# Kernel optimization log

Measured on AMD Instinct MI355X. Metric: run time of the kernel, lower is better.

The kernel has to match this reference:

```python
import jax, jax.numpy as jnp
import numpy as np

EPS = 1e-16  # PyG softmax eps
NEG_SLOPE = 0.2


def _gat_conv(x, W, att_src, att_dst, bias, src, dst, num_nodes, heads, ch, concat):
    # add self loops (PyG default add_self_loops=True)
    loop = jnp.arange(num_nodes, dtype=src.dtype)
    src = jnp.concatenate([src, loop])
    dst = jnp.concatenate([dst, loop])

    h = (x @ W).reshape(num_nodes, heads, ch)          # [N,H,C]
    a_src = jnp.sum(h * att_src, axis=-1)              # [N,H]
    a_dst = jnp.sum(h * att_dst, axis=-1)              # [N,H]

    e = a_src[src] + a_dst[dst]                        # [E,H]
    e = jnp.where(e > 0, e, NEG_SLOPE * e)             # leaky_relu

    # segment softmax over edges grouped by destination node
    m = jax.ops.segment_max(e, dst, num_segments=num_nodes)
    e = jnp.exp(e - m[dst])
    s = jax.ops.segment_sum(e, dst, num_segments=num_nodes)
    alpha = e / (s[dst] + EPS)                          # [E,H]

    msg = h[src] * alpha[:, :, None]                    # [E,H,C]
    out = jax.ops.segment_sum(msg, dst, num_segments=num_nodes)  # [N,H,C]

    if concat:
        out = out.reshape(num_nodes, heads * ch)
    else:
        out = out.mean(axis=1)
    return out + bias


def setup_inputs() -> dict:
    key = jax.random.key(0)
    ks = jax.random.split(key, 12)
    N, E = 50000, 800000
    C_in, C_hid, C_out, H = 128, 32, 64, 8

    x = jax.random.normal(ks[0], (N, C_in), dtype=jnp.float32)
    edge_index = jax.random.randint(ks[1], (2, E), 0, N, dtype=jnp.int64)
    edge_weight = jax.random.uniform(ks[2], (E,), dtype=jnp.float32)

    g = lambda k, shape, fan: jax.random.normal(k, shape, dtype=jnp.float32) * (1.0 / np.sqrt(fan))
    W1 = g(ks[3], (C_in, H * C_hid), C_in)
    att_src1 = g(ks[4], (H, C_hid), C_hid)
    att_dst1 = g(ks[5], (H, C_hid), C_hid)
    bias1 = jnp.zeros((H * C_hid,), dtype=jnp.float32)
    W2 = g(ks[6], (H * C_hid, C_out), H * C_hid)
    att_src2 = g(ks[7], (1, C_out), C_out)
    att_dst2 = g(ks[8], (1, C_out), C_out)
    bias2 = jnp.zeros((C_out,), dtype=jnp.float32)

    return {"x": x, "edge_index": edge_index, "edge_weight": edge_weight,
            "W1": W1, "att_src1": att_src1, "att_dst1": att_dst1, "bias1": bias1,
            "W2": W2, "att_src2": att_src2, "att_dst2": att_dst2, "bias2": bias2}


def reference(x, edge_index, edge_weight, W1, att_src1, att_dst1, bias1,
              W2, att_src2, att_dst2, bias2):
    N = x.shape[0]
    src, dst = edge_index[0], edge_index[1]
    # edge_weight is ignored: GATConv has edge_dim=None, so edge_attr contributes nothing
    h = _gat_conv(x, W1, att_src1, att_dst1, bias1, src, dst, N, 8, 32, concat=True)
    h = jax.nn.elu(h)
    out = _gat_conv(h, W2, att_src2, att_dst2, bias2, src, dst, N, 1, 64, concat=False)
    return out
```

## Files before the change

kernel.cpp:

```cpp
#include <hip/hip_runtime.h>
#include <hip/hip_fp16.h>
#include <math.h>


#define LEAKY(e) ((e) > 0.f ? (e) : 0.2f * (e))
#define CAP 64
#define NPART 4
#define NPB 12500
#define NPW 6250
#define CS 8192

struct __align__(8) H4 { __half2 a, b; };

typedef _Float16 half8 __attribute__((ext_vector_type(8)));
typedef float f32x4 __attribute__((ext_vector_type(4)));

__global__ __launch_bounds__(256) void k1_kernel(
    const int* __restrict__ ei, unsigned* __restrict__ Hg,
    const float* __restrict__ x,
    const float* __restrict__ W1, _Float16* __restrict__ h1h,
    const float* __restrict__ att_src1, const float* __restrict__ att_dst1,
    float* __restrict__ a_src1, float* __restrict__ a_dst1, int N, int E,
    int B, int hblocks) {
  __shared__ __align__(16) unsigned sraw[8704];
  int t = threadIdx.x, b = blockIdx.x;
  if (b < hblocks) {
    int chunk = b >> 2, p = b & 3;
    for (int i = t; i < NPW; i += 256) sraw[i] = 0u;
    __syncthreads();
    int base = chunk * CS;
    int pbase = p * NPB;
    if ((E & 3) == 0) {
      for (int j = 0; j < CS; j += 1024) {
        int idx = base + j + t * 4;
        if (idx < E) {
          int4 dv = *(const int4*)(ei + E + idx);
          unsigned dl;
          dl = (unsigned)(dv.x - pbase);
          if (dl < NPB) atomicAdd(&sraw[dl >> 1], 1u << ((dl & 1) * 16));
          dl = (unsigned)(dv.y - pbase);
          if (dl < NPB) atomicAdd(&sraw[dl >> 1], 1u << ((dl & 1) * 16));
          dl = (unsigned)(dv.z - pbase);
          if (dl < NPB) atomicAdd(&sraw[dl >> 1], 1u << ((dl & 1) * 16));
          dl = (unsigned)(dv.w - pbase);
          if (dl < NPB) atomicAdd(&sraw[dl >> 1], 1u << ((dl & 1) * 16));
        }
      }
    } else {
      for (int j = 0; j < CS; j += 256) {
        int idx = base + j + t;
        if (idx < E) {
          int d = ei[E + idx];
          unsigned dl = (unsigned)(d - pbase);
          if (dl < NPB) atomicAdd(&sraw[dl >> 1], 1u << ((dl & 1) * 16));
        }
      }
    }
    __syncthreads();
    unsigned* Hs = Hg + (size_t)(p * B + chunk) * NPW;
    for (int i = t; i < NPW; i += 256) Hs[i] = sraw[i];
    return;
  }
  _Float16* Bs = (_Float16*)sraw;
  int bx = b - hblocks;
  int cb = bx & 1;
  int c0 = cb * 128;
  int w = t >> 6, l = t & 63;
  int lm = l & 15, lq = l >> 4;
  {
    int n = t & 127;
    int kw = t >> 7;
#pragma unroll 8
    for (int i = 0; i < 64; i++) {
      int k = i * 2 + kw;
      Bs[n * 136 + k] = (_Float16)W1[k * 256 + c0 + n];
    }
  }
  __syncthreads();
  int m0 = (bx >> 1) * 128 + w * 32;
  int ra = m0 + lm;      if (ra > N - 1) ra = N - 1;
  int rb = m0 + 16 + lm; if (rb > N - 1) rb = N - 1;
  f32x4 acc[2][8];
#pragma unroll
  for (int mt = 0; mt < 2; mt++)
#pragma unroll
    for (int nt = 0; nt < 8; nt++) acc[mt][nt] = (f32x4){0.f, 0.f, 0.f, 0.f};
  for (int k0 = 0; k0 < 128; k0 += 32) {
    const float* pa = x + (size_t)ra * 128 + k0 + lq * 8;
    const float* pb = x + (size_t)rb * 128 + k0 + lq * 8;
    float4 u0 = *(const float4*)pa, u1 = *(const float4*)(pa + 4);
    float4 w0 = *(const float4*)pb, w1 = *(const float4*)(pb + 4);
    half8 a0, a1;
    a0[0] = (_Float16)u0.x; a0[1] = (_Float16)u0.y;
    a0[2] = (_Float16)u0.z; a0[3] = (_Float16)u0.w;
    a0[4] = (_Float16)u1.x; a0[5] = (_Float16)u1.y;
    a0[6] = (_Float16)u1.z; a0[7] = (_Float16)u1.w;
    a1[0] = (_Float16)w0.x; a1[1] = (_Float16)w0.y;
    a1[2] = (_Float16)w0.z; a1[3] = (_Float16)w0.w;
    a1[4] = (_Float16)w1.x; a1[5] = (_Float16)w1.y;
    a1[6] = (_Float16)w1.z; a1[7] = (_Float16)w1.w;
#pragma unroll
    for (int nt = 0; nt < 8; nt++) {
      half8 bv = *(const half8*)(Bs + (nt * 16 + lm) * 136 + k0 + lq * 8);
      acc[0][nt] = __builtin_amdgcn_mfma_f32_16x16x32_f16(a0, bv, acc[0][nt], 0, 0, 0);
      acc[1][nt] = __builtin_amdgcn_mfma_f32_16x16x32_f16(a1, bv, acc[1][nt], 0, 0, 0);
    }
  }
  float as_[8], ad_[8];
#pragma unroll
  for (int nt = 0; nt < 8; nt++) {
    as_[nt] = att_src1[c0 + nt * 16 + lm];
    ad_[nt] = att_dst1[c0 + nt * 16 + lm];
  }
#pragma unroll
  for (int mt = 0; mt < 2; mt++) {
#pragma unroll
    for (int i = 0; i < 4; i++) {
      int gr = m0 + mt * 16 + lq * 4 + i;
      bool ok = gr < N;
      if (ok) {
#pragma unroll
        for (int nt = 0; nt < 8; nt++)
          h1h[(size_t)gr * 256 + c0 + nt * 16 + lm] = (_Float16)acc[mt][nt][i];
      }
      float ph[4], qh[4];
#pragma unroll
      for (int hb = 0; hb < 4; hb++) {
        ph[hb] = acc[mt][2 * hb][i] * as_[2 * hb] +
                 acc[mt][2 * hb + 1][i] * as_[2 * hb + 1];
        qh[hb] = acc[mt][2 * hb][i] * ad_[2 * hb] +
                 acc[mt][2 * hb + 1][i] * ad_[2 * hb + 1];
      }
#pragma unroll
      for (int o = 1; o < 16; o <<= 1) {
#pragma unroll
        for (int hb = 0; hb < 4; hb++) {
          ph[hb] += __shfl_xor(ph[hb], o, 64);
          qh[hb] += __shfl_xor(qh[hb], o, 64);
        }
      }
      if (lm == 0 && ok) {
        int h0 = cb * 4;
#pragma unroll
        for (int hb = 0; hb < 4; hb++) {
          a_src1[(size_t)gr * 8 + h0 + hb] = ph[hb];
          a_dst1[(size_t)gr * 8 + h0 + hb] = qh[hb];
        }
      }
    }
  }
}

__global__ __launch_bounds__(256) void prefix_kernel(
    unsigned* __restrict__ Hg, int* __restrict__ deg,
    int* __restrict__ csr_src, int N, int B) {
  int wid = blockIdx.x * 256 + threadIdx.x;
  if (wid >= NPART * NPW) return;
  int p = wid / NPW, w0 = wid - p * NPW;
  unsigned* Hp = Hg + (size_t)p * B * NPW + w0;
  unsigned lo = 0, hi = 0;
  int b = 0;
  for (; b + 4 <= B; b += 4) {
    unsigned v0 = Hp[(size_t)(b + 0) * NPW];
    unsigned v1 = Hp[(size_t)(b + 1) * NPW];
    unsigned v2 = Hp[(size_t)(b + 2) * NPW];
    unsigned v3 = Hp[(size_t)(b + 3) * NPW];
    Hp[(size_t)(b + 0) * NPW] = lo | (hi << 16); lo += v0 & 0xffffu; hi += v0 >> 16;
    Hp[(size_t)(b + 1) * NPW] = lo | (hi << 16); lo += v1 & 0xffffu; hi += v1 >> 16;
    Hp[(size_t)(b + 2) * NPW] = lo | (hi << 16); lo += v2 & 0xffffu; hi += v2 >> 16;
    Hp[(size_t)(b + 3) * NPW] = lo | (hi << 16); lo += v3 & 0xffffu; hi += v3 >> 16;
  }
  for (; b < B; b++) {
    unsigned v = Hp[(size_t)b * NPW];
    Hp[(size_t)b * NPW] = lo | (hi << 16);
    lo += v & 0xffffu;
    hi += v >> 16;
  }
  int d0 = p * NPB + 2 * w0, d1 = d0 + 1;
  if (d0 < N) { deg[d0] = (int)lo; csr_src[(size_t)d0 * CAP] = d0; }
  if (d1 < N) { deg[d1] = (int)hi; csr_src[(size_t)d1 * CAP] = d1; }
}

__global__ __launch_bounds__(256) void scatter_kernel(
    const int* __restrict__ ei, const unsigned* __restrict__ Hg,
    int* __restrict__ csr_src, int E, int B) {
  __shared__ unsigned cnt[NPW];
  int t = threadIdx.x, b = blockIdx.x;
  int chunk = b >> 2, p = b & 3;
  const unsigned* Hs = Hg + (size_t)(p * B + chunk) * NPW;
  for (int i = t; i < NPW; i += 256) cnt[i] = Hs[i];
  __syncthreads();
  int base = chunk * CS;
  int pbase = p * NPB;
  if ((E & 3) == 0) {
    for (int j = 0; j < CS; j += 1024) {
      int idx = base + j + t * 4;
      if (idx < E) {
        int4 sv = *(const int4*)(ei + idx);
        int4 dv = *(const int4*)(ei + E + idx);
        int ss[4] = {sv.x, sv.y, sv.z, sv.w};
        int dd[4] = {dv.x, dv.y, dv.z, dv.w};
#pragma unroll
        for (int q = 0; q < 4; q++) {
          unsigned dl = (unsigned)(dd[q] - pbase);
          if (dl < NPB) {
            unsigned sh = (dl & 1) * 16;
            unsigned old = atomicAdd(&cnt[dl >> 1], 1u << sh);
            int slot = 1 + (int)((old >> sh) & 0xffffu);
            if (slot < CAP) csr_src[(size_t)dd[q] * CAP + slot] = ss[q];
          }
        }
      }
    }
  } else {
    for (int j = 0; j < CS; j += 256) {
      int idx = base + j + t;
      if (idx < E) {
        int s = ei[idx];
        int d = ei[E + idx];
        unsigned dl = (unsigned)(d - pbase);
        if (dl < NPB) {
          unsigned sh = (dl & 1) * 16;
          unsigned old = atomicAdd(&cnt[dl >> 1], 1u << sh);
          int slot = 1 + (int)((old >> sh) & 0xffffu);
          if (slot < CAP) csr_src[(size_t)d * CAP + slot] = s;
        }
      }
    }
  }
}

__global__ __launch_bounds__(256) void agg1_kernel(
    const int* __restrict__ deg, const int* __restrict__ csr_src,
    const float* __restrict__ a_src1, const float* __restrict__ a_dst1,
    const __half* __restrict__ h1h, const float* __restrict__ bias,
    _Float16* __restrict__ h_act, int n) {
  int w = threadIdx.x >> 6, l = threadIdx.x & 63;
  int d = blockIdx.x * 4 + w;
  if (d >= n) return;
  int cnt = deg[d] + 1;
  if (cnt > CAP) cnt = CAP;
  const int* sp = csr_src + (size_t)d * CAP;
  int hh = l >> 3;
  float adst = a_dst1[(size_t)d * 8 + hh];
  float4 acc = make_float4(0.f, 0.f, 0.f, 0.f);
  float p = 0.f;
  int i = 0;
  for (; i + 8 <= cnt; i += 8) {
    int s[8];
#pragma unroll
    for (int j = 0; j < 8; j++) s[j] = sp[i + j];
    int sm = sp[i + (l & 7)];
    float e = a_src1[(size_t)sm * 8 + hh] + adst;
    e = LEAKY(e);
    float ex = __expf(e);
    H4 v[8];
#pragma unroll
    for (int j = 0; j < 8; j++)
      v[j] = *(const H4*)(h1h + (size_t)s[j] * 256 + 4 * l);
    float xv[8];
#pragma unroll
    for (int j = 0; j < 8; j++) {
      xv[j] = __shfl(ex, (l & 56) + j, 64);
      p += xv[j];
    }
#pragma unroll
    for (int j = 0; j < 8; j++) {
      float2 p0 = __half22float2(v[j].a), p1 = __half22float2(v[j].b);
      acc.x = fmaf(p0.x, xv[j], acc.x);
      acc.y = fmaf(p0.y, xv[j], acc.y);
      acc.z = fmaf(p1.x, xv[j], acc.z);
      acc.w = fmaf(p1.y, xv[j], acc.w);
    }
  }
  for (; i < cnt; i++) {
    int s = sp[i];
    float e = a_src1[(size_t)s * 8 + hh] + adst;
    e = LEAKY(e);
    float a = __expf(e);
    p += a;
    H4 v = *(const H4*)(h1h + (size_t)s * 256 + 4 * l);
    float2 p0 = __half22float2(v.a), p1 = __half22float2(v.b);
    acc.x = fmaf(p0.x, a, acc.x);
    acc.y = fmaf(p0.y, a, acc.y);
    acc.z = fmaf(p1.x, a, acc.z);
    acc.w = fmaf(p1.y, a, acc.w);
  }
  float rinv = 1.f / (p + 1e-16f);
  float4 b = *(const float4*)(bias + 4 * l);
  float ox = fmaf(acc.x, rinv, b.x), oy = fmaf(acc.y, rinv, b.y);
  float oz = fmaf(acc.z, rinv, b.z), ow = fmaf(acc.w, rinv, b.w);
  ox = ox > 0.f ? ox : expm1f(ox);
  oy = oy > 0.f ? oy : expm1f(oy);
  oz = oz > 0.f ? oz : expm1f(oz);
  ow = ow > 0.f ? ow : expm1f(ow);
  H4 hv;
  hv.a = __floats2half2_rn(ox, oy);
  hv.b = __floats2half2_rn(oz, ow);
  *(H4*)(h_act + (size_t)d * 256 + 4 * l) = hv;
}

__global__ __launch_bounds__(256) void gemm2_kernel(
    const _Float16* __restrict__ h_act, const float* __restrict__ W2,
    _Float16* __restrict__ h2h, const float* __restrict__ att_src2,
    const float* __restrict__ att_dst2, float* __restrict__ a_src2,
    float* __restrict__ a_dst2, int N) {
  __shared__ _Float16 Bs[64 * 264];
  int t = threadIdx.x;
  int w = t >> 6, l = t & 63;
  int lm = l & 15, lq = l >> 4;
  {
    int n = t & 63;
    int kw = t >> 6;
#pragma unroll 8
    for (int i = 0; i < 64; i++) {
      int k = i * 4 + kw;
      Bs[n * 264 + k] = (_Float16)W2[k * 64 + n];
    }
  }
  __syncthreads();
  const int K = 256;
  int m0 = blockIdx.x * 128 + w * 32;
  int ra = m0 + lm;      if (ra > N - 1) ra = N - 1;
  int rb = m0 + 16 + lm; if (rb > N - 1) rb = N - 1;
  f32x4 acc[2][4];
#pragma unroll
  for (int mt = 0; mt < 2; mt++)
#pragma unroll
    for (int nt = 0; nt < 4; nt++) acc[mt][nt] = (f32x4){0.f, 0.f, 0.f, 0.f};
  for (int k0 = 0; k0 < K; k0 += 32) {
    half8 a0 = *(const half8*)(h_act + (size_t)ra * K + k0 + lq * 8);
    half8 a1 = *(const half8*)(h_act + (size_t)rb * K + k0 + lq * 8);
    half8 b0 = *(const half8*)(Bs + (0 + lm) * 264 + k0 + lq * 8);
    half8 b1 = *(const half8*)(Bs + (16 + lm) * 264 + k0 + lq * 8);
    half8 b2 = *(const half8*)(Bs + (32 + lm) * 264 + k0 + lq * 8);
    half8 b3 = *(const half8*)(Bs + (48 + lm) * 264 + k0 + lq * 8);
    acc[0][0] = __builtin_amdgcn_mfma_f32_16x16x32_f16(a0, b0, acc[0][0], 0, 0, 0);
    acc[0][1] = __builtin_amdgcn_mfma_f32_16x16x32_f16(a0, b1, acc[0][1], 0, 0, 0);
    acc[0][2] = __builtin_amdgcn_mfma_f32_16x16x32_f16(a0, b2, acc[0][2], 0, 0, 0);
    acc[0][3] = __builtin_amdgcn_mfma_f32_16x16x32_f16(a0, b3, acc[0][3], 0, 0, 0);
    acc[1][0] = __builtin_amdgcn_mfma_f32_16x16x32_f16(a1, b0, acc[1][0], 0, 0, 0);
    acc[1][1] = __builtin_amdgcn_mfma_f32_16x16x32_f16(a1, b1, acc[1][1], 0, 0, 0);
    acc[1][2] = __builtin_amdgcn_mfma_f32_16x16x32_f16(a1, b2, acc[1][2], 0, 0, 0);
    acc[1][3] = __builtin_amdgcn_mfma_f32_16x16x32_f16(a1, b3, acc[1][3], 0, 0, 0);
  }
  float as_[4], ad_[4];
#pragma unroll
  for (int nt = 0; nt < 4; nt++) {
    as_[nt] = att_src2[nt * 16 + lm];
    ad_[nt] = att_dst2[nt * 16 + lm];
  }
#pragma unroll
  for (int mt = 0; mt < 2; mt++) {
#pragma unroll
    for (int i = 0; i < 4; i++) {
      int gr = m0 + mt * 16 + lq * 4 + i;
      bool ok = gr < N;
      if (ok) {
#pragma unroll
        for (int nt = 0; nt < 4; nt++)
          h2h[(size_t)gr * 64 + nt * 16 + lm] = (_Float16)acc[mt][nt][i];
      }
      float p0 = acc[mt][0][i] * as_[0] + acc[mt][1][i] * as_[1];
      float p1 = acc[mt][2][i] * as_[2] + acc[mt][3][i] * as_[3];
      float q0 = acc[mt][0][i] * ad_[0] + acc[mt][1][i] * ad_[1];
      float q1 = acc[mt][2][i] * ad_[2] + acc[mt][3][i] * ad_[3];
#pragma unroll
      for (int o = 1; o < 16; o <<= 1) {
        p0 += __shfl_xor(p0, o, 64);
        p1 += __shfl_xor(p1, o, 64);
        q0 += __shfl_xor(q0, o, 64);
        q1 += __shfl_xor(q1, o, 64);
      }
      if (lm == 0 && ok) {
        a_src2[gr] = p0 + p1;
        a_dst2[gr] = q0 + q1;
      }
    }
  }
}

__global__ __launch_bounds__(256) void agg2_kernel(
    const int* __restrict__ deg, const int* __restrict__ csr_src,
    const float* __restrict__ a_src2, const float* __restrict__ a_dst2,
    const __half* __restrict__ h2h, const float* __restrict__ bias,
    float* __restrict__ out, int n) {
  int w = threadIdx.x >> 6, l = threadIdx.x & 63;
  int d = blockIdx.x * 4 + w;
  if (d >= n) return;
  int cnt = deg[d] + 1;
  if (cnt > CAP) cnt = CAP;
  const int* sp = csr_src + (size_t)d * CAP;
  float adst = a_dst2[d];
  int e2 = l >> 5;
  int c2 = (l & 31) * 2;
  float2 acc = make_float2(0.f, 0.f);
  float p = 0.f;
  int i = 0;
  for (; i + 16 <= cnt; i += 16) {
    int s[8];
#pragma unroll
    for (int j = 0; j < 8; j++) s[j] = sp[i + j * 2 + e2];
    int sm = sp[i + (l & 15)];
    float e = a_src2[sm] + adst;
    e = LEAKY(e);
    float ex = __expf(e);
    __half2 v[8];
#pragma unroll
    for (int j = 0; j < 8; j++)
      v[j] = *(const __half2*)(h2h + (size_t)s[j] * 64 + c2);
    float xv[8];
#pragma unroll
    for (int j = 0; j < 8; j++) {
      xv[j] = __shfl(ex, (l & 48) + j * 2 + e2, 64);
      p += xv[j];
    }
#pragma unroll
    for (int j = 0; j < 8; j++) {
      float2 f = __half22float2(v[j]);
      acc.x = fmaf(f.x, xv[j], acc.x);
      acc.y = fmaf(f.y, xv[j], acc.y);
    }
  }
  for (; i + e2 < cnt; i += 2) {
    int s = sp[i + e2];
    float e = a_src2[s] + adst;
    e = LEAKY(e);
    float a = __expf(e);
    p += a;
    float2 f = __half22float2(*(const __half2*)(h2h + (size_t)s * 64 + c2));
    acc.x = fmaf(f.x, a, acc.x);
    acc.y = fmaf(f.y, a, acc.y);
  }
  acc.x += __shfl_xor(acc.x, 32, 64);
  acc.y += __shfl_xor(acc.y, 32, 64);
  p += __shfl_xor(p, 32, 64);
  if (l < 32) {
    float rinv = 1.f / (p + 1e-16f);
    float2 b = *(const float2*)(bias + c2);
    *(float2*)(out + (size_t)d * 64 + c2) =
        make_float2(fmaf(acc.x, rinv, b.x), fmaf(acc.y, rinv, b.y));
  }
}

extern "C" void kernel_launch(void* const* d_in, const int* in_sizes, int n_in,
                              void* d_out, int out_size, void* d_ws, size_t ws_size,
                              hipStream_t stream) {
  const float* x        = (const float*)d_in[0];
  const int*   ei       = (const int*)d_in[1];
  const float* W1       = (const float*)d_in[3];
  const float* att_src1 = (const float*)d_in[4];
  const float* att_dst1 = (const float*)d_in[5];
  const float* bias1    = (const float*)d_in[6];
  const float* W2       = (const float*)d_in[7];
  const float* att_src2 = (const float*)d_in[8];
  const float* att_dst2 = (const float*)d_in[9];
  const float* bias2    = (const float*)d_in[10];
  float* out = (float*)d_out;

  int N = in_sizes[0] / 128;
  int E = in_sizes[1] / 2;
  int B = (E + CS - 1) / CS;
  int hblocks = B * NPART;

  char* ws = (char*)d_ws;
  size_t off = 0;
  auto carve = [&](size_t bytes) -> void* {
    void* p = ws + off;
    off += (bytes + 255) & ~(size_t)255;
    return p;
  };
  _Float16* h1h   = (_Float16*)carve((size_t)N * 256 * 2);
  _Float16* h2h   = (_Float16*)carve((size_t)N * 64 * 2);
  _Float16* h_act = (_Float16*)carve((size_t)N * 256 * 2);
  unsigned* Hg    = (unsigned*)carve((size_t)NPART * B * NPW * 4);
  float* a_src1  = (float*)carve((size_t)N * 8 * 4);
  float* a_dst1  = (float*)carve((size_t)N * 8 * 4);
  float* a_src2  = (float*)carve((size_t)N * 4);
  float* a_dst2  = (float*)carve((size_t)N * 4);
  int* deg       = (int*)carve((size_t)N * 4);
  int* csr_src   = (int*)carve((size_t)N * CAP * 4);
  (void)ws_size; (void)n_in; (void)out_size;

  int gblocks = ((N + 127) / 128) * 2;
  k1_kernel<<<hblocks + gblocks, 256, 0, stream>>>(
      ei, Hg, x, W1, h1h, att_src1, att_dst1, a_src1, a_dst1, N, E, B,
      hblocks);
  int pwords = NPART * NPW;
  prefix_kernel<<<(pwords + 255) / 256, 256, 0, stream>>>(Hg, deg, csr_src, N, B);
  scatter_kernel<<<hblocks, 256, 0, stream>>>(ei, Hg, csr_src, E, B);
  agg1_kernel<<<(N + 3) / 4, 256, 0, stream>>>(
      deg, csr_src, a_src1, a_dst1, (const __half*)h1h, bias1, h_act, N);
  gemm2_kernel<<<(N + 127) / 128, 256, 0, stream>>>(
      h_act, W2, h2h, att_src2, att_dst2, a_src2, a_dst2, N);
  agg2_kernel<<<(N + 3) / 4, 256, 0, stream>>>(
      deg, csr_src, a_src2, a_dst2, (const __half*)h2h, bias2, out, N);
}
```

Baseline: 256.3 us.

## Fuse layer-1 aggregation with layer-2 GEMM and attention logits

Merges agg1 and gemm2 into a single kernel. Each block aggregates 16 destination rows into shared memory after the ELU, then runs an MFMA against W2 staged in LDS and reduces the attention dot products through shared memory. This drops the h_act round trip to global memory and one kernel launch. In exchange, every block now re-stages the full W2 matrix into LDS (about 3125 blocks instead of about 391), and each block needs more LDS, which may lower occupancy.

```diff
diff --git a/kernel.cpp b/kernel.cpp
--- a/kernel.cpp
+++ b/kernel.cpp
@@ -234,148 +234,122 @@
     const int* __restrict__ deg, const int* __restrict__ csr_src,
     const float* __restrict__ a_src1, const float* __restrict__ a_dst1,
     const __half* __restrict__ h1h, const float* __restrict__ bias,
-    _Float16* __restrict__ h_act, int n) {
-  int w = threadIdx.x >> 6, l = threadIdx.x & 63;
-  int d = blockIdx.x * 4 + w;
-  if (d >= n) return;
-  int cnt = deg[d] + 1;
-  if (cnt > CAP) cnt = CAP;
-  const int* sp = csr_src + (size_t)d * CAP;
-  int hh = l >> 3;
-  float adst = a_dst1[(size_t)d * 8 + hh];
-  float4 acc = make_float4(0.f, 0.f, 0.f, 0.f);
-  float p = 0.f;
-  int i = 0;
-  for (; i + 8 <= cnt; i += 8) {
-    int s[8];
-#pragma unroll
-    for (int j = 0; j < 8; j++) s[j] = sp[i + j];
-    int sm = sp[i + (l & 7)];
-    float e = a_src1[(size_t)sm * 8 + hh] + adst;
-    e = LEAKY(e);
-    float ex = __expf(e);
-    H4 v[8];
-#pragma unroll
-    for (int j = 0; j < 8; j++)
-      v[j] = *(const H4*)(h1h + (size_t)s[j] * 256 + 4 * l);
-    float xv[8];
-#pragma unroll
-    for (int j = 0; j < 8; j++) {
-      xv[j] = __shfl(ex, (l & 56) + j, 64);
-      p += xv[j];
-    }
-#pragma unroll
-    for (int j = 0; j < 8; j++) {
-      float2 p0 = __half22float2(v[j].a), p1 = __half22float2(v[j].b);
-      acc.x = fmaf(p0.x, xv[j], acc.x);
-      acc.y = fmaf(p0.y, xv[j], acc.y);
-      acc.z = fmaf(p1.x, xv[j], acc.z);
-      acc.w = fmaf(p1.y, xv[j], acc.w);
-    }
-  }
-  for (; i < cnt; i++) {
-    int s = sp[i];
-    float e = a_src1[(size_t)s * 8 + hh] + adst;
-    e = LEAKY(e);
-    float a = __expf(e);
-    p += a;
-    H4 v = *(const H4*)(h1h + (size_t)s * 256 + 4 * l);
-    float2 p0 = __half22float2(v.a), p1 = __half22float2(v.b);
-    acc.x = fmaf(p0.x, a, acc.x);
-    acc.y = fmaf(p0.y, a, acc.y);
-    acc.z = fmaf(p1.x, a, acc.z);
-    acc.w = fmaf(p1.y, a, acc.w);
-  }
-  float rinv = 1.f / (p + 1e-16f);
-  float4 b = *(const float4*)(bias + 4 * l);
-  float ox = fmaf(acc.x, rinv, b.x), oy = fmaf(acc.y, rinv, b.y);
-  float oz = fmaf(acc.z, rinv, b.z), ow = fmaf(acc.w, rinv, b.w);
-  ox = ox > 0.f ? ox : expm1f(ox);
-  oy = oy > 0.f ? oy : expm1f(oy);
-  oz = oz > 0.f ? oz : expm1f(oz);
-  ow = ow > 0.f ? ow : expm1f(ow);
-  H4 hv;
-  hv.a = __floats2half2_rn(ox, oy);
-  hv.b = __floats2half2_rn(oz, ow);
-  *(H4*)(h_act + (size_t)d * 256 + 4 * l) = hv;
-}
-
-__global__ __launch_bounds__(256) void gemm2_kernel(
-    const _Float16* __restrict__ h_act, const float* __restrict__ W2,
-    _Float16* __restrict__ h2h, const float* __restrict__ att_src2,
-    const float* __restrict__ att_dst2, float* __restrict__ a_src2,
-    float* __restrict__ a_dst2, int N) {
+    const float* __restrict__ W2, const float* __restrict__ att_src2,
+    const float* __restrict__ att_dst2, _Float16* __restrict__ h2h,
+    float* __restrict__ a_src2, float* __restrict__ a_dst2, int n) {
   __shared__ _Float16 Bs[64 * 264];
+  __shared__ _Float16 Ls[16 * 264];
+  __shared__ float psum[4][16], qsum[4][16];
   int t = threadIdx.x;
   int w = t >> 6, l = t & 63;
-  int lm = l & 15, lq = l >> 4;
   {
-    int n = t & 63;
-    int kw = t >> 6;
+    int c = t & 63, kw = t >> 6;
 #pragma unroll 8
     for (int i = 0; i < 64; i++) {
       int k = i * 4 + kw;
-      Bs[n * 264 + k] = (_Float16)W2[k * 64 + n];
-    }
+      Bs[c * 264 + k] = (_Float16)W2[k * 64 + c];
+    }
+  }
+  int hh = l >> 3;
+  float4 bb = *(const float4*)(bias + 4 * l);
+  for (int it = 0; it < 4; it++) {
+    int row = it * 4 + w;
+    int d = blockIdx.x * 16 + row;
+    H4 hv;
+    if (d < n) {
+      int cnt = deg[d] + 1;
+      if (cnt > CAP) cnt = CAP;
+      const int* sp = csr_src + (size_t)d * CAP;
+      float adst = a_dst1[(size_t)d * 8 + hh];
+      float4 acc = make_float4(0.f, 0.f, 0.f, 0.f);
+      float p = 0.f;
+      int i = 0;
+      for (; i + 8 <= cnt; i += 8) {
+        int s[8];
+#pragma unroll
+        for (int j = 0; j < 8; j++) s[j] = sp[i + j];
+        int sm = sp[i + (l & 7)];
+        float e = a_src1[(size_t)sm * 8 + hh] + adst;
+        e = LEAKY(e);
+        float ex = __expf(e);
+        H4 v[8];
+#pragma unroll
+        for (int j = 0; j < 8; j++)
+          v[j] = *(const H4*)(h1h + (size_t)s[j] * 256 + 4 * l);
+        float xv[8];
+#pragma unroll
+        for (int j = 0; j < 8; j++) {
+          xv[j] = __shfl(ex, (l & 56) + j, 64);
+          p += xv[j];
+        }
+#pragma unroll
+        for (int j = 0; j < 8; j++) {
+          float2 p0 = __half22float2(v[j].a), p1 = __half22float2(v[j].b);
+          acc.x = fmaf(p0.x, xv[j], acc.x);
+          acc.y = fmaf(p0.y, xv[j], acc.y);
+          acc.z = fmaf(p1.x, xv[j], acc.z);
+          acc.w = fmaf(p1.y, xv[j], acc.w);
+        }
+      }
+      for (; i < cnt; i++) {
+        int s = sp[i];
+        float e = a_src1[(size_t)s * 8 + hh] + adst;
+        e = LEAKY(e);
+        float a = __expf(e);
+        p += a;
+        H4 v = *(const H4*)(h1h + (size_t)s * 256 + 4 * l);
+        float2 p0 = __half22float2(v.a), p1 = __half22float2(v.b);
+        acc.x = fmaf(p0.x, a, acc.x);
+        acc.y = fmaf(p0.y, a, acc.y);
+        acc.z = fmaf(p1.x, a, acc.z);
+        acc.w = fmaf(p1.y, a, acc.w);
+      }
+      float rinv = 1.f / (p + 1e-16f);
+      float ox = fmaf(acc.x, rinv, bb.x), oy = fmaf(acc.y, rinv, bb.y);
+      float oz = fmaf(acc.z, rinv, bb.z), ow = fmaf(acc.w, rinv, bb.w);
+      ox = ox > 0.f ? ox : expm1f(ox);
+      oy = oy > 0.f ? oy : expm1f(oy);
+      oz = oz > 0.f ? oz : expm1f(oz);
+      ow = ow > 0.f ? ow : expm1f(ow);
+      hv.a = __floats2half2_rn(ox, oy);
+      hv.b = __floats2half2_rn(oz, ow);
+    } else {
+      hv.a = __floats2half2_rn(0.f, 0.f);
+      hv.b = __floats2half2_rn(0.f, 0.f);
+    }
+    *(H4*)(Ls + row * 264 + 4 * l) = hv;
   }
   __syncthreads();
-  const int K = 256;
-  int m0 = blockIdx.x * 128 + w * 32;
-  int ra = m0 + lm;      if (ra > N - 1) ra = N - 1;
-  int rb = m0 + 16 + lm; if (rb > N - 1) rb = N - 1;
-  f32x4 acc[2][4];
-#pragma unroll
-  for (int mt = 0; mt < 2; mt++)
-#pragma unroll
-    for (int nt = 0; nt < 4; nt++) acc[mt][nt] = (f32x4){0.f, 0.f, 0.f, 0.f};
-  for (int k0 = 0; k0 < K; k0 += 32) {
-    half8 a0 = *(const half8*)(h_act + (size_t)ra * K + k0 + lq * 8);
-    half8 a1 = *(const half8*)(h_act + (size_t)rb * K + k0 + lq * 8);
-    half8 b0 = *(const half8*)(Bs + (0 + lm) * 264 + k0 + lq * 8);
-    half8 b1 = *(const half8*)(Bs + (16 + lm) * 264 + k0 + lq * 8);
-    half8 b2 = *(const half8*)(Bs + (32 + lm) * 264 + k0 + lq * 8);
-    half8 b3 = *(const half8*)(Bs + (48 + lm) * 264 + k0 + lq * 8);
-    acc[0][0] = __builtin_amdgcn_mfma_f32_16x16x32_f16(a0, b0, acc[0][0], 0, 0, 0);
-    acc[0][1] = __builtin_amdgcn_mfma_f32_16x16x32_f16(a0, b1, acc[0][1], 0, 0, 0);
-    acc[0][2] = __builtin_amdgcn_mfma_f32_16x16x32_f16(a0, b2, acc[0][2], 0, 0, 0);
-    acc[0][3] = __builtin_amdgcn_mfma_f32_16x16x32_f16(a0, b3, acc[0][3], 0, 0, 0);
-    acc[1][0] = __builtin_amdgcn_mfma_f32_16x16x32_f16(a1, b0, acc[1][0], 0, 0, 0);
-    acc[1][1] = __builtin_amdgcn_mfma_f32_16x16x32_f16(a1, b1, acc[1][1], 0, 0, 0);
-    acc[1][2] = __builtin_amdgcn_mfma_f32_16x16x32_f16(a1, b2, acc[1][2], 0, 0, 0);
-    acc[1][3] = __builtin_amdgcn_mfma_f32_16x16x32_f16(a1, b3, acc[1][3], 0, 0, 0);
-  }
-  float as_[4], ad_[4];
-#pragma unroll
-  for (int nt = 0; nt < 4; nt++) {
-    as_[nt] = att_src2[nt * 16 + lm];
-    ad_[nt] = att_dst2[nt * 16 + lm];
-  }
-#pragma unroll
-  for (int mt = 0; mt < 2; mt++) {
-#pragma unroll
-    for (int i = 0; i < 4; i++) {
-      int gr = m0 + mt * 16 + lq * 4 + i;
-      bool ok = gr < N;
-      if (ok) {
-#pragma unroll
-        for (int nt = 0; nt < 4; nt++)
-          h2h[(size_t)gr * 64 + nt * 16 + lm] = (_Float16)acc[mt][nt][i];
-      }
-      float p0 = acc[mt][0][i] * as_[0] + acc[mt][1][i] * as_[1];
-      float p1 = acc[mt][2][i] * as_[2] + acc[mt][3][i] * as_[3];
-      float q0 = acc[mt][0][i] * ad_[0] + acc[mt][1][i] * ad_[1];
-      float q1 = acc[mt][2][i] * ad_[2] + acc[mt][3][i] * ad_[3];
-#pragma unroll
-      for (int o = 1; o < 16; o <<= 1) {
-        p0 += __shfl_xor(p0, o, 64);
-        p1 += __shfl_xor(p1, o, 64);
-        q0 += __shfl_xor(q0, o, 64);
-        q1 += __shfl_xor(q1, o, 64);
-      }
-      if (lm == 0 && ok) {
-        a_src2[gr] = p0 + p1;
-        a_dst2[gr] = q0 + q1;
-      }
+  int lm = l & 15, lq = l >> 4;
+  f32x4 acc2 = (f32x4){0.f, 0.f, 0.f, 0.f};
+  for (int k0 = 0; k0 < 256; k0 += 32) {
+    half8 av = *(const half8*)(Ls + lm * 264 + k0 + lq * 8);
+    half8 bv = *(const half8*)(Bs + (w * 16 + lm) * 264 + k0 + lq * 8);
+    acc2 = __builtin_amdgcn_mfma_f32_16x16x32_f16(av, bv, acc2, 0, 0, 0);
+  }
+  float asv = att_src2[w * 16 + lm], adv = att_dst2[w * 16 + lm];
+#pragma unroll
+  for (int i = 0; i < 4; i++) {
+    int row = lq * 4 + i;
+    int d2 = blockIdx.x * 16 + row;
+    if (d2 < n) h2h[(size_t)d2 * 64 + w * 16 + lm] = (_Float16)acc2[i];
+    float pp = acc2[i] * asv, qq = acc2[i] * adv;
+#pragma unroll
+    for (int o = 1; o < 16; o <<= 1) {
+      pp += __shfl_xor(pp, o, 64);
+      qq += __shfl_xor(qq, o, 64);
+    }
+    if (lm == 0) {
+      psum[w][row] = pp;
+      qsum[w][row] = qq;
+    }
+  }
+  __syncthreads();
+  if (t < 16) {
+    int d2 = blockIdx.x * 16 + t;
+    if (d2 < n) {
+      a_src2[d2] = psum[0][t] + psum[1][t] + psum[2][t] + psum[3][t];
+      a_dst2[d2] = qsum[0][t] + qsum[1][t] + qsum[2][t] + qsum[3][t];
     }
   }
 }
@@ -472,7 +446,6 @@
   };
   _Float16* h1h   = (_Float16*)carve((size_t)N * 256 * 2);
   _Float16* h2h   = (_Float16*)carve((size_t)N * 64 * 2);
-  _Float16* h_act = (_Float16*)carve((size_t)N * 256 * 2);
   unsigned* Hg    = (unsigned*)carve((size_t)NPART * B * NPW * 4);
   float* a_src1  = (float*)carve((size_t)N * 8 * 4);
   float* a_dst1  = (float*)carve((size_t)N * 8 * 4);
@@ -489,10 +462,9 @@
   int pwords = NPART * NPW;
   prefix_kernel<<<(pwords + 255) / 256, 256, 0, stream>>>(Hg, deg, csr_src, N, B);
   scatter_kernel<<<hblocks, 256, 0, stream>>>(ei, Hg, csr_src, E, B);
-  agg1_kernel<<<(N + 3) / 4, 256, 0, stream>>>(
-      deg, csr_src, a_src1, a_dst1, (const __half*)h1h, bias1, h_act, N);
-  gemm2_kernel<<<(N + 127) / 128, 256, 0, stream>>>(
-      h_act, W2, h2h, att_src2, att_dst2, a_src2, a_dst2, N);
+  agg1_kernel<<<(N + 15) / 16, 256, 0, stream>>>(
+      deg, csr_src, a_src1, a_dst1, (const __half*)h1h, bias1, W2, att_src2,
+      att_dst2, h2h, a_src2, a_dst2, N);
   agg2_kernel<<<(N + 3) / 4, 256, 0, stream>>>(
       deg, csr_src, a_src2, a_dst2, (const __half*)h2h, bias2, out, N);
 }
```

Result: slower. 295.5 us (+15.3%).
